# Kernel optimization log

Measured on AMD Instinct MI355X. Metric: run time of the kernel, lower is better.

The kernel has to match this reference:

```python
import jax, jax.numpy as jnp
import numpy as np

DIM = 256
HEADS = 8
HEAD_DIM = DIM // HEADS
B = 4
Wd, Hd = 48, 48
N = Wd * Hd  # 2304


def _layernorm(x, g, b, eps=1e-5):
    mu = jnp.mean(x, axis=-1, keepdims=True)
    var = jnp.mean(jnp.square(x - mu), axis=-1, keepdims=True)
    return (x - mu) * jax.lax.rsqrt(var + eps) * g + b


def _build_mask(mask):
    # Binarize: <1 -> 0, >0 -> 1 (identity on {0,1} inputs)
    m = (mask > 0).astype(jnp.float32)
    flat = m.reshape(B, m.shape[1], Hd * Wd)[:, 0, :]  # [B, N]
    # mask[b,i,j] zeroed where (flat[j]==0 & flat[i]==1) | (flat[j]==0 & flat[i]==0)
    col0 = flat[:, None, :] == 0   # varies along j
    row = flat[:, :, None]         # varies along i
    bad = (col0 & (row == 1)) | (col0 & (row == 0))
    return (~bad).astype(jnp.float32)  # [B, N, N]


def setup_inputs() -> dict:
    key = jax.random.key(0)
    ks = jax.random.split(key, 12)
    s = 0.02
    x = jax.random.normal(ks[0], (B, N, DIM), jnp.float32)
    mask = jax.random.randint(ks[1], (B, 1, Wd, Hd), 0, 2).astype(jnp.float32)
    inp = {
        "x": x,
        "mask": mask,
        "ln_g": jnp.ones((DIM,), jnp.float32),
        "ln_b": jnp.zeros((DIM,), jnp.float32),
        "Wq": jax.random.normal(ks[2], (DIM, DIM), jnp.float32) * s,
        "bq": jnp.zeros((DIM,), jnp.float32),
        "Wk": jax.random.normal(ks[3], (DIM, DIM), jnp.float32) * s,
        "bk": jnp.zeros((DIM,), jnp.float32),
        "Wv": jax.random.normal(ks[4], (DIM, DIM), jnp.float32) * s,
        "bv": jnp.zeros((DIM,), jnp.float32),
        "Wp": jax.random.normal(ks[5], (DIM, DIM), jnp.float32) * s,
        "bp": jnp.zeros((DIM,), jnp.float32),
    }
    return inp


def reference(x, mask, ln_g, ln_b, Wq, bq, Wk, bk, Wv, bv, Wp, bp):
    Bx, Nx, C = x.shape
    mask_f = _build_mask(mask)  # [B, N, N]
    xn = _layernorm(x, ln_g, ln_b)
    def heads(Wm, bm):
        return (xn @ Wm + bm).reshape(Bx, Nx, HEADS, HEAD_DIM).transpose(0, 2, 1, 3)
    q = heads(Wq, bq)
    k = heads(Wk, bk)
    v = heads(Wv, bv)
    # NOTE: no 1/sqrt(d) scaling in the original; multiplicative 0/1 mask pre-softmax
    attn = jnp.einsum("bhnd,bhmd->bhnm", q, k) * mask_f[:, None, :, :]
    attn = jax.nn.softmax(attn, axis=-1)
    out = jnp.einsum("bhnm,bhmd->bhnd", attn, v)
    out = out.transpose(0, 2, 1, 3).reshape(Bx, Nx, C)
    return out @ Wp + bp
```

## Files before the change

kernel.cpp:

```cpp
#include <hip/hip_runtime.h>
#include <math.h>

typedef __attribute__((ext_vector_type(8))) short short8;
typedef __attribute__((ext_vector_type(4))) float f32x4;

constexpr int B   = 4;
constexpr int N   = 2304;
constexpr int DIM = 256;
constexpr int NH  = 8;
constexpr int DH  = 32;
constexpr int M   = B * N;
constexpr int SLOTS = 2336;
constexpr int CST = SLOTS * DH;

__device__ inline unsigned short f2bf(float f) {
    union { float f; unsigned u; } c; c.f = f;
    unsigned u = c.u;
    u += 0x7fffu + ((u >> 16) & 1u);
    return (unsigned short)(u >> 16);
}
__device__ inline unsigned short f2bf_trunc(float f) {
    union { float f; unsigned u; } c; c.f = f;
    return (unsigned short)(c.u >> 16);
}
__device__ inline float bf2f(unsigned short h) {
    union { unsigned u; float f; } c; c.u = ((unsigned)h) << 16;
    return c.f;
}

__device__ inline size_t fo256(int r, int k) {
    return ((size_t)((r >> 4) * 8 + (k >> 5)) << 9)
         + (size_t)(((((k & 31) >> 3) << 4) + (r & 15)) * 8 + (k & 7));
}
__device__ inline size_t foQK(int n, int d) {
    return ((size_t)(n >> 4) << 9)
         + (size_t)((((d >> 3) << 4) + (n & 15)) * 8 + (d & 7));
}
__device__ inline size_t foVTC(int d, int key) {
    return ((size_t)((d >> 4) * (SLOTS / 32) + (key >> 5)) << 9)
         + (size_t)(((((key & 31) >> 3) << 4) + (d & 15)) * 8 + (key & 7));
}

__global__ __launch_bounds__(256) void mask_scan(
    const float* __restrict__ mask, int* __restrict__ slotmap,
    int* __restrict__ ncp)
{
    __shared__ int wsum[4];
    int b = blockIdx.x, t = threadIdx.x;
    int wave = t >> 6, lane = t & 63;
    int cnt = 0;
    for (int j = t; j < N; j += 256) cnt += (mask[(size_t)b * N + j] > 0.f);
    #pragma unroll
    for (int o = 32; o > 0; o >>= 1) cnt += __shfl_down(cnt, o, 64);
    if (lane == 0) wsum[wave] = cnt;
    __syncthreads();
    int Nc = wsum[0] + wsum[1] + wsum[2] + wsum[3];
    int Nkp = (Nc + 31) & ~31;
    if (t == 0) { ncp[b * 2] = Nc; ncp[b * 2 + 1] = Nkp; }
    int baseK = 0;
    for (int j0 = 0; j0 < N; j0 += 256) {
        int j = j0 + t;
        bool keep = mask[(size_t)b * N + j] > 0.f;
        unsigned long long bal = __ballot(keep);
        int pos = __popcll(bal & ((1ull << lane) - 1ull));
        int wc  = __popcll(bal);
        __syncthreads();
        if (lane == 0) wsum[wave] = wc;
        __syncthreads();
        int wb = 0;
        for (int w = 0; w < wave; ++w) wb += wsum[w];
        int tot = wsum[0] + wsum[1] + wsum[2] + wsum[3];
        int keptBefore = baseK + wb + pos;
        slotmap[(size_t)b * N + j] = keep ? keptBefore : Nkp + (j - keptBefore);
        baseK += tot;
    }
}

__global__ __launch_bounds__(256) void ln_kernel(
    const float* __restrict__ x, const float* __restrict__ g,
    const float* __restrict__ bta,
    unsigned short* __restrict__ xh, unsigned short* __restrict__ xl)
{
    int tid = threadIdx.x;
    int wave = tid >> 6, lane = tid & 63;
    int row = blockIdx.x * 4 + wave;
    float4 v = *(const float4*)&x[(size_t)row * DIM + lane * 4];
    float s = v.x + v.y + v.z + v.w;
    #pragma unroll
    for (int o = 32; o > 0; o >>= 1) s += __shfl_xor(s, o, 64);
    float mu = s * (1.0f / DIM);
    float d0 = v.x - mu, d1 = v.y - mu, d2 = v.z - mu, d3 = v.w - mu;
    float s2 = d0 * d0 + d1 * d1 + d2 * d2 + d3 * d3;
    #pragma unroll
    for (int o = 32; o > 0; o >>= 1) s2 += __shfl_xor(s2, o, 64);
    float r = rsqrtf(s2 * (1.0f / DIM) + 1e-5f);
    float4 gg = *(const float4*)&g[lane * 4];
    float4 bb = *(const float4*)&bta[lane * 4];
    float y0 = d0 * r * gg.x + bb.x;
    float y1 = d1 * r * gg.y + bb.y;
    float y2 = d2 * r * gg.z + bb.z;
    float y3 = d3 * r * gg.w + bb.w;
    ushort4 hi, lo;
    hi.x = f2bf(y0); lo.x = f2bf(y0 - bf2f(hi.x));
    hi.y = f2bf(y1); lo.y = f2bf(y1 - bf2f(hi.y));
    hi.z = f2bf(y2); lo.z = f2bf(y2 - bf2f(hi.z));
    hi.w = f2bf(y3); lo.w = f2bf(y3 - bf2f(hi.w));
    size_t o = fo256(row, lane * 4);
    *(ushort4*)&xh[o] = hi;
    *(ushort4*)&xl[o] = lo;
}

__global__ __launch_bounds__(256) void split_w(
    const float* __restrict__ Wq, const float* __restrict__ Wk,
    const float* __restrict__ Wv, const float* __restrict__ Wp,
    unsigned short* __restrict__ Wth, unsigned short* __restrict__ Wtl)
{
    int z = blockIdx.z;
    const float* W = (z == 0) ? Wq : (z == 1) ? Wk : (z == 2) ? Wv : Wp;
    unsigned short* oh = Wth + (size_t)z * DIM * DIM;
    unsigned short* ol = Wtl + (size_t)z * DIM * DIM;
    __shared__ float t[32][33];
    int tid = threadIdx.x;
    int tx = tid & 31, ty0 = tid >> 5;
    int n0 = blockIdx.x * 32, k0 = blockIdx.y * 32;
    for (int ty = ty0; ty < 32; ty += 8)
        t[ty][tx] = W[(size_t)(k0 + ty) * DIM + n0 + tx];
    __syncthreads();
    for (int nn = ty0; nn < 32; nn += 8) {
        float v = t[tx][nn];
        unsigned short hh = f2bf(v);
        size_t o = fo256(n0 + nn, k0 + tx);
        oh[o] = hh;
        ol[o] = f2bf(v - bf2f(hh));
    }
}

__global__ __launch_bounds__(256, 4) void gemm_qkv(
    const unsigned short* __restrict__ Ahi, const unsigned short* __restrict__ Alo,
    const unsigned short* __restrict__ Wth, const unsigned short* __restrict__ Wtl,
    const float* __restrict__ bq, const float* __restrict__ bk,
    const float* __restrict__ bv, const int* __restrict__ slotmap,
    unsigned short* __restrict__ qb, unsigned short* __restrict__ kc,
    unsigned short* __restrict__ vc)
{
    int z = blockIdx.z;
    int bx = blockIdx.x;
    int tid = threadIdx.x;
    int wave = tid >> 6, lane = tid & 63;
    int quad = lane >> 4, l16 = lane & 15;
    const unsigned short* Whi = Wth + (size_t)z * DIM * DIM;
    const unsigned short* Wlo = Wtl + (size_t)z * DIM * DIM;
    int mrow0, ncol0;
    const unsigned short *Phi, *Plo, *Shi, *Slo;
    if (z < 2) {
        mrow0 = (bx >> 3) * 128 + wave * 32;
        ncol0 = (bx & 7) * 32;
        Phi = Ahi; Plo = Alo; Shi = Whi; Slo = Wlo;
    } else {
        mrow0 = (bx / 288) * 128 + wave * 32;
        ncol0 = (bx % 288) * 32;
        Phi = Whi; Plo = Wlo; Shi = Ahi; Slo = Alo;
    }
    f32x4 acc[2][2] = {};
    #pragma unroll
    for (int k0 = 0; k0 < DIM; k0 += 32) {
        size_t at = (((size_t)(mrow0 >> 4) * 8 + (k0 >> 5)) << 9) + lane * 8;
        size_t bt = (((size_t)(ncol0 >> 4) * 8 + (k0 >> 5)) << 9) + lane * 8;
        short8 ah0 = *(const short8*)&Phi[at];
        short8 al0 = *(const short8*)&Plo[at];
        short8 ah1 = *(const short8*)&Phi[at + 4096];
        short8 al1 = *(const short8*)&Plo[at + 4096];
        short8 bh0 = *(const short8*)&Shi[bt];
        short8 bl0 = *(const short8*)&Slo[bt];
        short8 bh1 = *(const short8*)&Shi[bt + 4096];
        short8 bl1 = *(const short8*)&Slo[bt + 4096];
        acc[0][0] = __builtin_amdgcn_mfma_f32_16x16x32_bf16(ah0, bh0, acc[0][0], 0, 0, 0);
        acc[0][0] = __builtin_amdgcn_mfma_f32_16x16x32_bf16(ah0, bl0, acc[0][0], 0, 0, 0);
        acc[0][0] = __builtin_amdgcn_mfma_f32_16x16x32_bf16(al0, bh0, acc[0][0], 0, 0, 0);
        acc[0][1] = __builtin_amdgcn_mfma_f32_16x16x32_bf16(ah0, bh1, acc[0][1], 0, 0, 0);
        acc[0][1] = __builtin_amdgcn_mfma_f32_16x16x32_bf16(ah0, bl1, acc[0][1], 0, 0, 0);
        acc[0][1] = __builtin_amdgcn_mfma_f32_16x16x32_bf16(al0, bh1, acc[0][1], 0, 0, 0);
        acc[1][0] = __builtin_amdgcn_mfma_f32_16x16x32_bf16(ah1, bh0, acc[1][0], 0, 0, 0);
        acc[1][0] = __builtin_amdgcn_mfma_f32_16x16x32_bf16(ah1, bl0, acc[1][0], 0, 0, 0);
        acc[1][0] = __builtin_amdgcn_mfma_f32_16x16x32_bf16(al1, bh0, acc[1][0], 0, 0, 0);
        acc[1][1] = __builtin_amdgcn_mfma_f32_16x16x32_bf16(ah1, bh1, acc[1][1], 0, 0, 0);
        acc[1][1] = __builtin_amdgcn_mfma_f32_16x16x32_bf16(ah1, bl1, acc[1][1], 0, 0, 0);
        acc[1][1] = __builtin_amdgcn_mfma_f32_16x16x32_bf16(al1, bh1, acc[1][1], 0, 0, 0);
    }
    if (z < 2) {
        const float* bias = z ? bk : bq;
        int b = mrow0 / N;
        int nbase = mrow0 - b * N;
        const int* smap = slotmap + (size_t)b * N;
        #pragma unroll
        for (int j = 0; j < 2; ++j) {
            int c = ncol0 + j * 16 + l16;
            int h = c >> 5, d = c & 31;
            float bs = bias[c];
            unsigned short* ob = z
                ? kc + (size_t)(b * NH + h) * CST
                : qb + (size_t)(b * NH + h) * ((size_t)N * DH);
            #pragma unroll
            for (int i = 0; i < 2; ++i)
            #pragma unroll
            for (int r = 0; r < 4; ++r) {
                int n = nbase + i * 16 + quad * 4 + r;
                int slot = z ? smap[n] : n;
                ob[foQK(slot, d)] = f2bf(acc[i][j][r] + bs);
            }
        }
    } else {
        int b = ncol0 / N;
        int kbase = ncol0 - b * N;
        const int* smap = slotmap + (size_t)b * N;
        #pragma unroll
        for (int i = 0; i < 2; ++i)
        #pragma unroll
        for (int r = 0; r < 4; ++r) {
            int m = mrow0 + i * 16 + quad * 4 + r;
            int h = m >> 5, d = m & 31;
            float bs = bv[m];
            unsigned short* ob = vc + (size_t)(b * NH + h) * CST;
            #pragma unroll
            for (int j = 0; j < 2; ++j) {
                int slot = smap[kbase + j * 16 + l16];
                ob[foVTC(d, slot)] = f2bf(acc[i][j][r] + bs);
            }
        }
    }
}

__global__ __launch_bounds__(256) void vmsum_kernel(
    const unsigned short* __restrict__ vc, const int* __restrict__ ncp,
    float* __restrict__ vm)
{
    int bh = blockIdx.x, b = bh >> 3;
    int tid = threadIdx.x;
    int wave = tid >> 6, lane = tid & 63;
    int kq = lane >> 4, l16 = lane & 15;
    int Nc = ncp[b * 2], Nkp = ncp[b * 2 + 1];
    int mend = Nkp + (N - Nc);
    int tbeg = Nkp >> 5, tend = (mend + 31) >> 5;
    int wgid = blockIdx.y * 4 + wave;
    const int WSTEP = 32;
    const unsigned short* vcb = vc + (size_t)bh * CST;
    #pragma unroll
    for (int dt = 0; dt < 2; ++dt) {
        float s = 0.f;
        for (int t = tbeg + wgid; t < tend; t += WSTEP) {
            short8 v = *(const short8*)&vcb[((size_t)(dt * (SLOTS / 32) + t) << 9) + lane * 8];
            int keyb = t * 32 + kq * 8;
            #pragma unroll
            for (int j = 0; j < 8; ++j)
                s += (keyb + j < mend) ? bf2f((unsigned short)v[j]) : 0.f;
        }
        s += __shfl_xor(s, 16, 64);
        s += __shfl_xor(s, 32, 64);
        if (lane < 16) atomicAdd(&vm[bh * 32 + dt * 16 + l16], s);
    }
}

__global__ __launch_bounds__(256, 4) void attn_kernel(
    const unsigned short* __restrict__ Qb,
    const unsigned short* __restrict__ Kc,
    const unsigned short* __restrict__ Vc,
    const int* __restrict__ ncp,
    float* __restrict__ po, float* __restrict__ pl)
{
    __shared__ unsigned short pbuf[8 * 16 * 40];
    int tid  = threadIdx.x;
    int wave = tid >> 6, lane = tid & 63;
    int quad = lane >> 4, l16 = lane & 15;
    int bh = blockIdx.y, b = bh >> 3;
    int sp = blockIdx.z;
    int q0 = (blockIdx.x * 4 + wave) * 32;

    const unsigned short* Qf = Qb + (size_t)bh * ((size_t)N * DH);
    const unsigned short* Kf = Kc + (size_t)bh * CST;
    const unsigned short* Vf = Vc + (size_t)bh * CST;

    int Nc  = ncp[b * 2];
    int Nkp = ncp[b * 2 + 1];
    int chunks = Nkp >> 5;
    int cbeg = sp ? (chunks >> 1) : 0;
    int cend = sp ? chunks : (chunks >> 1);
    int kbeg = cbeg << 5, kend = cend << 5;

    short8 qA0 = *(const short8*)&Qf[((size_t)(q0 >> 4) << 9) + lane * 8];
    short8 qA1 = *(const short8*)&Qf[((size_t)((q0 >> 4) + 1) << 9) + lane * 8];

    f32x4 o00 = {0,0,0,0}, o01 = {0,0,0,0}, o10 = {0,0,0,0}, o11 = {0,0,0,0};
    float l0[4] = {0,0,0,0}, l1[4] = {0,0,0,0};

    unsigned short* pb0 = &pbuf[(wave * 2 + 0) * 640];
    unsigned short* pb1 = &pbuf[(wave * 2 + 1) * 640];

    short8 kB0 = *(const short8*)&Kf[((size_t)(kbeg >> 4) << 9) + lane * 8];
    short8 kB1 = *(const short8*)&Kf[((size_t)((kbeg >> 4) + 1) << 9) + lane * 8];
    short8 vB0 = *(const short8*)&Vf[((size_t)(kbeg >> 5) << 9) + lane * 8];
    short8 vB1 = *(const short8*)&Vf[((size_t)((SLOTS / 32) + (kbeg >> 5)) << 9) + lane * 8];

    for (int k0 = kbeg; k0 < kend; k0 += 32) {
        int kn = (k0 + 32 < kend) ? k0 + 32 : kbeg;
        short8 nk0 = *(const short8*)&Kf[((size_t)(kn >> 4) << 9) + lane * 8];
        short8 nk1 = *(const short8*)&Kf[((size_t)((kn >> 4) + 1) << 9) + lane * 8];
        short8 nv0 = *(const short8*)&Vf[((size_t)(kn >> 5) << 9) + lane * 8];
        short8 nv1 = *(const short8*)&Vf[((size_t)((SLOTS / 32) + (kn >> 5)) << 9) + lane * 8];

        bool in0 = (k0 + l16) < Nc;
        bool in1 = (k0 + 16 + l16) < Nc;
        f32x4 z = {0,0,0,0};
        f32x4 s00 = __builtin_amdgcn_mfma_f32_16x16x32_bf16(qA0, kB0, z, 0, 0, 0);
        f32x4 s01 = __builtin_amdgcn_mfma_f32_16x16x32_bf16(qA0, kB1, z, 0, 0, 0);
        f32x4 s10 = __builtin_amdgcn_mfma_f32_16x16x32_bf16(qA1, kB0, z, 0, 0, 0);
        f32x4 s11 = __builtin_amdgcn_mfma_f32_16x16x32_bf16(qA1, kB1, z, 0, 0, 0);
        #pragma unroll
        for (int r = 0; r < 4; ++r) {
            int row = quad * 4 + r;
            float p00 = in0 ? __expf(s00[r]) : 0.f;
            float p01 = in1 ? __expf(s01[r]) : 0.f;
            float p10 = in0 ? __expf(s10[r]) : 0.f;
            float p11 = in1 ? __expf(s11[r]) : 0.f;
            l0[r] += p00 + p01;
            l1[r] += p10 + p11;
            pb0[row * 40 + l16]      = f2bf_trunc(p00);
            pb0[row * 40 + 16 + l16] = f2bf_trunc(p01);
            pb1[row * 40 + l16]      = f2bf_trunc(p10);
            pb1[row * 40 + 16 + l16] = f2bf_trunc(p11);
        }
        short8 pA0 = *(const short8*)&pb0[l16 * 40 + quad * 8];
        short8 pA1 = *(const short8*)&pb1[l16 * 40 + quad * 8];
        o00 = __builtin_amdgcn_mfma_f32_16x16x32_bf16(pA0, vB0, o00, 0, 0, 0);
        o01 = __builtin_amdgcn_mfma_f32_16x16x32_bf16(pA0, vB1, o01, 0, 0, 0);
        o10 = __builtin_amdgcn_mfma_f32_16x16x32_bf16(pA1, vB0, o10, 0, 0, 0);
        o11 = __builtin_amdgcn_mfma_f32_16x16x32_bf16(pA1, vB1, o11, 0, 0, 0);

        kB0 = nk0; kB1 = nk1; vB0 = nv0; vB1 = nv1;
    }
    #pragma unroll
    for (int r = 0; r < 4; ++r) {
        #pragma unroll
        for (int off = 1; off < 16; off <<= 1) {
            l0[r] += __shfl_xor(l0[r], off, 64);
            l1[r] += __shfl_xor(l1[r], off, 64);
        }
    }
    size_t pbase = (size_t)(bh * 2 + sp) * N;
    #pragma unroll
    for (int r = 0; r < 4; ++r) {
        int row = quad * 4 + r;
        size_t b0 = (pbase + q0 + row) * DH;
        size_t b1 = (pbase + q0 + 16 + row) * DH;
        po[b0 + l16]      = o00[r];
        po[b0 + 16 + l16] = o01[r];
        po[b1 + l16]      = o10[r];
        po[b1 + 16 + l16] = o11[r];
        if (l16 == 0) {
            pl[pbase + q0 + row]      = l0[r];
            pl[pbase + q0 + 16 + row] = l1[r];
        }
    }
}

__global__ __launch_bounds__(256) void combine_kernel(
    const float* __restrict__ po, const float* __restrict__ pl,
    const float* __restrict__ vm, const int* __restrict__ ncp,
    unsigned short* __restrict__ ahn_hi, unsigned short* __restrict__ ahn_lo)
{
    int idx = blockIdx.x * 256 + threadIdx.x;
    int bhq = idx >> 2;
    int dg  = (idx & 3) * 8;
    int bh = bhq / N, q = bhq - bh * N;
    int b = bh >> 3, h = bh & 7;
    size_t p0 = ((size_t)(bh * 2 + 0) * N + q) * DH + dg;
    size_t p1 = ((size_t)(bh * 2 + 1) * N + q) * DH + dg;
    int Nc = ncp[b * 2];
    float l = pl[(size_t)(bh * 2) * N + q] + pl[(size_t)(bh * 2 + 1) * N + q]
            + (float)(N - Nc);
    float inv = 1.f / l;
    float4 a0 = *(const float4*)&po[p0];
    float4 a1 = *(const float4*)&po[p0 + 4];
    float4 c0 = *(const float4*)&po[p1];
    float4 c1 = *(const float4*)&po[p1 + 4];
    float4 m0 = *(const float4*)&vm[bh * 32 + dg];
    float4 m1 = *(const float4*)&vm[bh * 32 + dg + 4];
    float vals[8] = {
        (a0.x + c0.x + m0.x) * inv, (a0.y + c0.y + m0.y) * inv,
        (a0.z + c0.z + m0.z) * inv, (a0.w + c0.w + m0.w) * inv,
        (a1.x + c1.x + m1.x) * inv, (a1.y + c1.y + m1.y) * inv,
        (a1.z + c1.z + m1.z) * inv, (a1.w + c1.w + m1.w) * inv };
    union { unsigned short u[8]; short8 v; } hi, lo;
    #pragma unroll
    for (int j = 0; j < 8; ++j) {
        unsigned short t = f2bf(vals[j]);
        hi.u[j] = t;
        lo.u[j] = f2bf(vals[j] - bf2f(t));
    }
    size_t o = fo256(b * N + q, h * 32 + dg);
    *(short8*)&ahn_hi[o] = hi.v;
    *(short8*)&ahn_lo[o] = lo.v;
}

__global__ __launch_bounds__(256, 4) void gemm_p(
    const unsigned short* __restrict__ Ahi, const unsigned short* __restrict__ Alo,
    const unsigned short* __restrict__ Wth, const unsigned short* __restrict__ Wtl,
    const float* __restrict__ bias, float* __restrict__ out)
{
    const unsigned short* Bhi = Wth + (size_t)3 * DIM * DIM;
    const unsigned short* Blo = Wtl + (size_t)3 * DIM * DIM;
    int tid = threadIdx.x;
    int wave = tid >> 6, lane = tid & 63;
    int quad = lane >> 4, l16 = lane & 15;
    int r0 = blockIdx.y * 128 + wave * 32;
    int c0 = blockIdx.x * 16;
    f32x4 acc0 = {}, acc1 = {};
    #pragma unroll
    for (int k0 = 0; k0 < DIM; k0 += 32) {
        size_t at = (((size_t)(r0 >> 4) * 8 + (k0 >> 5)) << 9) + lane * 8;
        size_t bt = (((size_t)(c0 >> 4) * 8 + (k0 >> 5)) << 9) + lane * 8;
        short8 ah0 = *(const short8*)&Ahi[at];
        short8 al0 = *(const short8*)&Alo[at];
        short8 ah1 = *(const short8*)&Ahi[at + 4096];
        short8 al1 = *(const short8*)&Alo[at + 4096];
        short8 bh = *(const short8*)&Bhi[bt];
        short8 bl = *(const short8*)&Blo[bt];
        acc0 = __builtin_amdgcn_mfma_f32_16x16x32_bf16(ah0, bh, acc0, 0, 0, 0);
        acc0 = __builtin_amdgcn_mfma_f32_16x16x32_bf16(ah0, bl, acc0, 0, 0, 0);
        acc0 = __builtin_amdgcn_mfma_f32_16x16x32_bf16(al0, bh, acc0, 0, 0, 0);
        acc1 = __builtin_amdgcn_mfma_f32_16x16x32_bf16(ah1, bh, acc1, 0, 0, 0);
        acc1 = __builtin_amdgcn_mfma_f32_16x16x32_bf16(ah1, bl, acc1, 0, 0, 0);
        acc1 = __builtin_amdgcn_mfma_f32_16x16x32_bf16(al1, bh, acc1, 0, 0, 0);
    }
    int c = c0 + l16;
    float bs = bias[c];
    #pragma unroll
    for (int r = 0; r < 4; ++r) {
        int R0 = r0 + quad * 4 + r;
        out[(size_t)R0 * DIM + c] = acc0[r] + bs;
        out[(size_t)(R0 + 16) * DIM + c] = acc1[r] + bs;
    }
}

extern "C" void kernel_launch(void* const* d_in, const int* in_sizes, int n_in,
                              void* d_out, int out_size, void* d_ws, size_t ws_size,
                              hipStream_t stream)
{
    const float* x    = (const float*)d_in[0];
    const float* mask = (const float*)d_in[1];
    const float* ln_g = (const float*)d_in[2];
    const float* ln_b = (const float*)d_in[3];
    const float* Wq   = (const float*)d_in[4];
    const float* bq   = (const float*)d_in[5];
    const float* Wk   = (const float*)d_in[6];
    const float* bk   = (const float*)d_in[7];
    const float* Wv   = (const float*)d_in[8];
    const float* bv   = (const float*)d_in[9];
    const float* Wp   = (const float*)d_in[10];
    const float* bp   = (const float*)d_in[11];
    float* out = (float*)d_out;

    constexpr size_t SZ  = (size_t)M * DIM;
    constexpr size_t CSZ = (size_t)B * NH * CST;
    constexpr size_t WSZ = (size_t)DIM * DIM;
    unsigned short* p = (unsigned short*)d_ws;
    unsigned short* xh = p;  p += SZ;
    unsigned short* xl = p;  p += SZ;
    unsigned short* qb = p;  p += SZ;
    unsigned short* kc = p;  p += CSZ;
    unsigned short* vc = p;  p += CSZ;
    unsigned short* ah = p;  p += SZ;
    unsigned short* al = p;  p += SZ;
    unsigned short* wth = p; p += 4 * WSZ;
    unsigned short* wtl = p; p += 4 * WSZ;
    float* po = (float*)p;
    float* pl = po + (size_t)B * NH * 2 * N * DH;
    float* vm = pl + (size_t)B * NH * 2 * N;
    int* slotmap = (int*)(vm + (size_t)B * NH * 32);
    int* ncp = slotmap + (size_t)B * N;

    mask_scan<<<B, 256, 0, stream>>>(mask, slotmap, ncp);

    ln_kernel<<<M / 4, 256, 0, stream>>>(x, ln_g, ln_b, xh, xl);

    split_w<<<dim3(8, 8, 4), 256, 0, stream>>>(Wq, Wk, Wv, Wp, wth, wtl);

    gemm_qkv<<<dim3(576, 1, 3), 256, 0, stream>>>(
        xh, xl, wth, wtl, bq, bk, bv, slotmap, qb, kc, vc);

    hipMemsetAsync(vm, 0, (size_t)B * NH * 32 * sizeof(float), stream);
    vmsum_kernel<<<dim3(B * NH, 8), 256, 0, stream>>>(vc, ncp, vm);

    attn_kernel<<<dim3(N / 128, B * NH, 2), 256, 0, stream>>>(
        qb, kc, vc, ncp, po, pl);

    combine_kernel<<<(B * NH * N * 4) / 256, 256, 0, stream>>>(
        po, pl, vm, ncp, ah, al);

    gemm_p<<<dim3(DIM / 16, M / 128), 256, 0, stream>>>(
        ah, al, wth, wtl, bp, out);
}
```

Baseline: 175.2 us.

## Gather normalized x into slot order before QKV GEMM; write K/V contiguously

The mask scan now writes an inverse slot-to-token map and zeroes the vm buffer, which replaces a separate memset. A new permute_x kernel gathers the split bf16 LayerNorm output into slot order with zeroed pad rows. The K and V GEMMs then read the permuted activations and write contiguous slot-ordered outputs instead of scattering through slotmap, and the K path skips row tiles beyond the padded kept count. This adds an extra kernel and a workspace copy of x in exchange for coalesced stores and less K work. The vmsum masking changes to sum only the non-kept region, to match the new zero-padded layout.

```diff
diff --git a/kernel.cpp b/kernel.cpp
--- a/kernel.cpp
+++ b/kernel.cpp
@@ -12,6 +12,7 @@
 constexpr int M   = B * N;
 constexpr int SLOTS = 2336;
 constexpr int CST = SLOTS * DH;
+constexpr int XPB = SLOTS * DIM;
 
 __device__ inline unsigned short f2bf(float f) {
     union { float f; unsigned u; } c; c.f = f;
@@ -42,12 +43,13 @@
 }
 
 __global__ __launch_bounds__(256) void mask_scan(
-    const float* __restrict__ mask, int* __restrict__ slotmap,
-    int* __restrict__ ncp)
+    const float* __restrict__ mask, int* __restrict__ inv,
+    int* __restrict__ ncp, float* __restrict__ vm)
 {
     __shared__ int wsum[4];
     int b = blockIdx.x, t = threadIdx.x;
     int wave = t >> 6, lane = t & 63;
+    vm[b * 256 + t] = 0.f;
     int cnt = 0;
     for (int j = t; j < N; j += 256) cnt += (mask[(size_t)b * N + j] > 0.f);
     #pragma unroll
@@ -71,7 +73,8 @@
         for (int w = 0; w < wave; ++w) wb += wsum[w];
         int tot = wsum[0] + wsum[1] + wsum[2] + wsum[3];
         int keptBefore = baseK + wb + pos;
-        slotmap[(size_t)b * N + j] = keep ? keptBefore : Nkp + (j - keptBefore);
+        if (keep) inv[(size_t)b * SLOTS + keptBefore] = j;
+        else      inv[(size_t)b * SLOTS + Nkp + (j - keptBefore)] = j;
         baseK += tot;
     }
 }
@@ -135,45 +138,91 @@
     }
 }
 
+__global__ __launch_bounds__(256) void permute_x(
+    const unsigned short* __restrict__ xh, const unsigned short* __restrict__ xl,
+    const int* __restrict__ inv, const int* __restrict__ ncp,
+    unsigned short* __restrict__ xph, unsigned short* __restrict__ xpl)
+{
+    int tid = threadIdx.x;
+    int wave = tid >> 6, lane = tid & 63;
+    int kq = lane >> 4, r = lane & 15;
+    int rtg = blockIdx.x * 4 + wave;
+    int b = rtg / (SLOTS / 16), rt = rtg % (SLOTS / 16);
+    int y = blockIdx.y;
+    const unsigned short* src = (y & 1) ? xl : xh;
+    unsigned short* dst = ((y & 1) ? xpl : xph) + (size_t)b * XPB;
+    int slot = rt * 16 + r;
+    int Nc = ncp[b * 2], Nkp = ncp[b * 2 + 1];
+    int mend = Nkp + (N - Nc);
+    bool pad = (slot >= Nc && slot < Nkp) || slot >= mend;
+    int n = pad ? -1 : inv[(size_t)b * SLOTS + slot];
+    #pragma unroll
+    for (int kt = 0; kt < 4; ++kt) {
+        int k0 = ((y >> 1) * 4 + kt) * 32;
+        short8 v = {0, 0, 0, 0, 0, 0, 0, 0};
+        if (n >= 0) {
+            int gn = b * N + n;
+            v = *(const short8*)&src[(((size_t)(gn >> 4) * 8 + (k0 >> 5)) << 9)
+                                     + (kq * 16 + (gn & 15)) * 8];
+        }
+        *(short8*)&dst[(((size_t)(rt * 8 + (k0 >> 5))) << 9) + lane * 8] = v;
+    }
+}
+
 __global__ __launch_bounds__(256, 4) void gemm_qkv(
-    const unsigned short* __restrict__ Ahi, const unsigned short* __restrict__ Alo,
+    const unsigned short* __restrict__ xh, const unsigned short* __restrict__ xl,
+    const unsigned short* __restrict__ xph, const unsigned short* __restrict__ xpl,
     const unsigned short* __restrict__ Wth, const unsigned short* __restrict__ Wtl,
     const float* __restrict__ bq, const float* __restrict__ bk,
-    const float* __restrict__ bv, const int* __restrict__ slotmap,
+    const float* __restrict__ bv, const int* __restrict__ ncp,
     unsigned short* __restrict__ qb, unsigned short* __restrict__ kc,
     unsigned short* __restrict__ vc)
 {
-    int z = blockIdx.z;
-    int bx = blockIdx.x;
+    constexpr size_t WSZ = (size_t)DIM * DIM;
+    int z = blockIdx.z, bx = blockIdx.x;
     int tid = threadIdx.x;
     int wave = tid >> 6, lane = tid & 63;
     int quad = lane >> 4, l16 = lane & 15;
-    const unsigned short* Whi = Wth + (size_t)z * DIM * DIM;
-    const unsigned short* Wlo = Wtl + (size_t)z * DIM * DIM;
-    int mrow0, ncol0;
-    const unsigned short *Phi, *Plo, *Shi, *Slo;
-    if (z < 2) {
-        mrow0 = (bx >> 3) * 128 + wave * 32;
-        ncol0 = (bx & 7) * 32;
-        Phi = Ahi; Plo = Alo; Shi = Whi; Slo = Wlo;
+    const unsigned short *PAh, *PAl, *PBh, *PBl;
+    int arow0, brow0, b;
+    if (z == 0) {
+        if (bx >= 576) return;
+        arow0 = (bx >> 3) * 128 + wave * 32;
+        brow0 = (bx & 7) * 32;
+        b = ((bx >> 3) * 128) / N;
+        PAh = xh; PAl = xl;
+        PBh = Wth; PBl = Wtl;
+    } else if (z == 1) {
+        b = bx / 152;
+        int rr = bx % 152;
+        arow0 = (rr >> 3) * 128 + wave * 32;
+        brow0 = (rr & 7) * 32;
+        if (arow0 >= SLOTS) return;
+        if (arow0 >= ncp[b * 2 + 1]) return;
+        PAh = xph + (size_t)b * XPB; PAl = xpl + (size_t)b * XPB;
+        PBh = Wth + WSZ; PBl = Wtl + WSZ;
     } else {
-        mrow0 = (bx / 288) * 128 + wave * 32;
-        ncol0 = (bx % 288) * 32;
-        Phi = Whi; Plo = Wlo; Shi = Ahi; Slo = Alo;
+        if (bx >= 584) return;
+        int nidx = bx % 292;
+        b = nidx / 73;
+        arow0 = (bx / 292) * 128 + wave * 32;
+        brow0 = (nidx % 73) * 32;
+        PAh = Wth + 2 * WSZ; PAl = Wtl + 2 * WSZ;
+        PBh = xph + (size_t)b * XPB; PBl = xpl + (size_t)b * XPB;
     }
     f32x4 acc[2][2] = {};
     #pragma unroll
     for (int k0 = 0; k0 < DIM; k0 += 32) {
-        size_t at = (((size_t)(mrow0 >> 4) * 8 + (k0 >> 5)) << 9) + lane * 8;
-        size_t bt = (((size_t)(ncol0 >> 4) * 8 + (k0 >> 5)) << 9) + lane * 8;
-        short8 ah0 = *(const short8*)&Phi[at];
-        short8 al0 = *(const short8*)&Plo[at];
-        short8 ah1 = *(const short8*)&Phi[at + 4096];
-        short8 al1 = *(const short8*)&Plo[at + 4096];
-        short8 bh0 = *(const short8*)&Shi[bt];
-        short8 bl0 = *(const short8*)&Slo[bt];
-        short8 bh1 = *(const short8*)&Shi[bt + 4096];
-        short8 bl1 = *(const short8*)&Slo[bt + 4096];
+        size_t at = (((size_t)(arow0 >> 4) * 8 + (k0 >> 5)) << 9) + lane * 8;
+        size_t bt = (((size_t)(brow0 >> 4) * 8 + (k0 >> 5)) << 9) + lane * 8;
+        short8 ah0 = *(const short8*)&PAh[at];
+        short8 al0 = *(const short8*)&PAl[at];
+        short8 ah1 = *(const short8*)&PAh[at + 4096];
+        short8 al1 = *(const short8*)&PAl[at + 4096];
+        short8 bh0 = *(const short8*)&PBh[bt];
+        short8 bl0 = *(const short8*)&PBl[bt];
+        short8 bh1 = *(const short8*)&PBh[bt + 4096];
+        short8 bl1 = *(const short8*)&PBl[bt + 4096];
         acc[0][0] = __builtin_amdgcn_mfma_f32_16x16x32_bf16(ah0, bh0, acc[0][0], 0, 0, 0);
         acc[0][0] = __builtin_amdgcn_mfma_f32_16x16x32_bf16(ah0, bl0, acc[0][0], 0, 0, 0);
         acc[0][0] = __builtin_amdgcn_mfma_f32_16x16x32_bf16(al0, bh0, acc[0][0], 0, 0, 0);
@@ -187,44 +236,50 @@
         acc[1][1] = __builtin_amdgcn_mfma_f32_16x16x32_bf16(ah1, bl1, acc[1][1], 0, 0, 0);
         acc[1][1] = __builtin_amdgcn_mfma_f32_16x16x32_bf16(al1, bh1, acc[1][1], 0, 0, 0);
     }
-    if (z < 2) {
-        const float* bias = z ? bk : bq;
-        int b = mrow0 / N;
-        int nbase = mrow0 - b * N;
-        const int* smap = slotmap + (size_t)b * N;
+    if (z == 0) {
+        int nbase = arow0 - b * N;
         #pragma unroll
         for (int j = 0; j < 2; ++j) {
-            int c = ncol0 + j * 16 + l16;
+            int c = brow0 + j * 16 + l16;
             int h = c >> 5, d = c & 31;
-            float bs = bias[c];
-            unsigned short* ob = z
-                ? kc + (size_t)(b * NH + h) * CST
-                : qb + (size_t)(b * NH + h) * ((size_t)N * DH);
+            float bs = bq[c];
+            unsigned short* ob = qb + (size_t)(b * NH + h) * ((size_t)N * DH);
             #pragma unroll
             for (int i = 0; i < 2; ++i)
             #pragma unroll
             for (int r = 0; r < 4; ++r) {
                 int n = nbase + i * 16 + quad * 4 + r;
-                int slot = z ? smap[n] : n;
+                ob[foQK(n, d)] = f2bf(acc[i][j][r] + bs);
+            }
+        }
+    } else if (z == 1) {
+        #pragma unroll
+        for (int j = 0; j < 2; ++j) {
+            int c = brow0 + j * 16 + l16;
+            int h = c >> 5, d = c & 31;
+            float bs = bk[c];
+            unsigned short* ob = kc + (size_t)(b * NH + h) * CST;
+            #pragma unroll
+            for (int i = 0; i < 2; ++i)
+            #pragma unroll
+            for (int r = 0; r < 4; ++r) {
+                int slot = arow0 + i * 16 + quad * 4 + r;
                 ob[foQK(slot, d)] = f2bf(acc[i][j][r] + bs);
             }
         }
     } else {
-        int b = ncol0 / N;
-        int kbase = ncol0 - b * N;
-        const int* smap = slotmap + (size_t)b * N;
         #pragma unroll
         for (int i = 0; i < 2; ++i)
         #pragma unroll
         for (int r = 0; r < 4; ++r) {
-            int m = mrow0 + i * 16 + quad * 4 + r;
+            int m = arow0 + i * 16 + quad * 4 + r;
             int h = m >> 5, d = m & 31;
             float bs = bv[m];
             unsigned short* ob = vc + (size_t)(b * NH + h) * CST;
             #pragma unroll
             for (int j = 0; j < 2; ++j) {
-                int slot = smap[kbase + j * 16 + l16];
-                ob[foVTC(d, slot)] = f2bf(acc[i][j][r] + bs);
+                int key = brow0 + j * 16 + l16;
+                ob[foVTC(d, key)] = f2bf(acc[i][j][r] + bs);
             }
         }
     }
@@ -252,7 +307,7 @@
             int keyb = t * 32 + kq * 8;
             #pragma unroll
             for (int j = 0; j < 8; ++j)
-                s += (keyb + j < mend) ? bf2f((unsigned short)v[j]) : 0.f;
+                s += (keyb + j >= Nkp && keyb + j < mend) ? bf2f((unsigned short)v[j]) : 0.f;
         }
         s += __shfl_xor(s, 16, 64);
         s += __shfl_xor(s, 32, 64);
@@ -406,8 +461,9 @@
     const unsigned short* __restrict__ Wth, const unsigned short* __restrict__ Wtl,
     const float* __restrict__ bias, float* __restrict__ out)
 {
-    const unsigned short* Bhi = Wth + (size_t)3 * DIM * DIM;
-    const unsigned short* Blo = Wtl + (size_t)3 * DIM * DIM;
+    constexpr size_t WSZ = (size_t)DIM * DIM;
+    const unsigned short* Bhi = Wth + 3 * WSZ;
+    const unsigned short* Blo = Wtl + 3 * WSZ;
     int tid = threadIdx.x;
     int wave = tid >> 6, lane = tid & 63;
     int quad = lane >> 4, l16 = lane & 15;
@@ -461,10 +517,13 @@
 
     constexpr size_t SZ  = (size_t)M * DIM;
     constexpr size_t CSZ = (size_t)B * NH * CST;
+    constexpr size_t XSZ = (size_t)B * XPB;
     constexpr size_t WSZ = (size_t)DIM * DIM;
     unsigned short* p = (unsigned short*)d_ws;
     unsigned short* xh = p;  p += SZ;
     unsigned short* xl = p;  p += SZ;
+    unsigned short* xph = p; p += XSZ;
+    unsigned short* xpl = p; p += XSZ;
     unsigned short* qb = p;  p += SZ;
     unsigned short* kc = p;  p += CSZ;
     unsigned short* vc = p;  p += CSZ;
@@ -475,19 +534,21 @@
     float* po = (float*)p;
     float* pl = po + (size_t)B * NH * 2 * N * DH;
     float* vm = pl + (size_t)B * NH * 2 * N;
-    int* slotmap = (int*)(vm + (size_t)B * NH * 32);
-    int* ncp = slotmap + (size_t)B * N;
-
-    mask_scan<<<B, 256, 0, stream>>>(mask, slotmap, ncp);
+    int* inv = (int*)(vm + (size_t)B * NH * 32);
+    int* ncp = inv + (size_t)B * SLOTS;
+
+    mask_scan<<<B, 256, 0, stream>>>(mask, inv, ncp, vm);
 
     ln_kernel<<<M / 4, 256, 0, stream>>>(x, ln_g, ln_b, xh, xl);
 
     split_w<<<dim3(8, 8, 4), 256, 0, stream>>>(Wq, Wk, Wv, Wp, wth, wtl);
 
-    gemm_qkv<<<dim3(576, 1, 3), 256, 0, stream>>>(
-        xh, xl, wth, wtl, bq, bk, bv, slotmap, qb, kc, vc);
-
-    hipMemsetAsync(vm, 0, (size_t)B * NH * 32 * sizeof(float), stream);
+    permute_x<<<dim3((B * (SLOTS / 16)) / 4, 4), 256, 0, stream>>>(
+        xh, xl, inv, ncp, xph, xpl);
+
+    gemm_qkv<<<dim3(608, 1, 3), 256, 0, stream>>>(
+        xh, xl, xph, xpl, wth, wtl, bq, bk, bv, ncp, qb, kc, vc);
+
     vmsum_kernel<<<dim3(B * NH, 8), 256, 0, stream>>>(vc, ncp, vm);
 
     attn_kernel<<<dim3(N / 128, B * NH, 2), 256, 0, stream>>>(
```

Result: slower. 179.5 us (+2.5%).
